# Optimization experiments

Hardware: AMD Instinct MI355X
Metric: run time of the kernel (lower is better)

The kernel has to match this reference:

```python
import jax, jax.numpy as jnp
import numpy as np

V, E, HD, T = 32000, 100, 256, 17   # vocab, embed dim, lstm hidden (bidir total), tagset
B, S = 64, 1024
H = HD // 2                         # per-direction hidden


def setup_inputs() -> dict:
    key = jax.random.key(0)
    ks = jax.random.split(key, 16)
    p = lambda k, sh: (jax.random.normal(k, sh, jnp.float32) * 0.1)
    sentence = jax.random.randint(ks[0], (B, S), 0, V)
    mask = jnp.ones((B, S), dtype=bool)
    embed = p(ks[1], (V, E)).at[0].set(0.0)  # padding_idx=0
    inp = {
        "sentence": sentence,
        "mask": mask,
        "embed": embed,
        "w_ih_f": p(ks[2], (4 * H, E)), "w_hh_f": p(ks[3], (4 * H, H)),
        "b_ih_f": p(ks[4], (4 * H,)), "b_hh_f": p(ks[5], (4 * H,)),
        "w_ih_b": p(ks[6], (4 * H, E)), "w_hh_b": p(ks[7], (4 * H, H)),
        "b_ih_b": p(ks[8], (4 * H,)), "b_hh_b": p(ks[9], (4 * H,)),
        "fc_w": p(ks[10], (T, HD)), "fc_b": p(ks[11], (T,)),
        "start_trans": p(ks[12], (T,)),
        "end_trans": p(ks[13], (T,)),
        "trans": p(ks[14], (T, T)),
    }
    return inp


def _lstm_dir(xs, w_ih, w_hh, b_ih, b_hh):
    # xs: [S, B, E] -> hs: [S, B, H]. PyTorch gate order: i, f, g, o.
    xg = jnp.einsum('sbe,ge->sbg', xs, w_ih) + b_ih  # precompute input projections
    h0 = jnp.zeros((xs.shape[1], H), xs.dtype)
    def step(carry, xg_t):
        h, c = carry
        g = xg_t + h @ w_hh.T + b_hh
        i, f, gg, o = jnp.split(g, 4, axis=-1)
        c = jax.nn.sigmoid(f) * c + jax.nn.sigmoid(i) * jnp.tanh(gg)
        h = jax.nn.sigmoid(o) * jnp.tanh(c)
        return (h, c), h
    _, hs = jax.lax.scan(step, (h0, h0), xg)
    return hs


def _emissions(sentence, embed, w_ih_f, w_hh_f, b_ih_f, b_hh_f,
               w_ih_b, w_hh_b, b_ih_b, b_hh_b, fc_w, fc_b):
    x = embed[sentence]                      # [B, S, E] (dropout is identity in eval)
    xs = x.transpose(1, 0, 2)                # [S, B, E]
    hf = _lstm_dir(xs, w_ih_f, w_hh_f, b_ih_f, b_hh_f)
    hb = _lstm_dir(xs[::-1], w_ih_b, w_hh_b, b_ih_b, b_hh_b)[::-1]
    hcat = jnp.concatenate([hf, hb], axis=-1)            # [S, B, 2H]
    return jnp.einsum('sbh,th->sbt', hcat, fc_w) + fc_b  # [S, B, T]


def reference(sentence, mask, embed, w_ih_f, w_hh_f, b_ih_f, b_hh_f,
              w_ih_b, w_hh_b, b_ih_b, b_hh_b, fc_w, fc_b,
              start_trans, end_trans, trans):
    em = _emissions(sentence, embed, w_ih_f, w_hh_f, b_ih_f, b_hh_f,
                    w_ih_b, w_hh_b, b_ih_b, b_hh_b, fc_w, fc_b)  # [S, B, T]
    mk = mask.T  # [S, B]

    # Viterbi forward pass (max-plus recurrence over the tagset)
    score0 = start_trans + em[0]  # [B, T]
    def vstep(score, inp):
        emit_t, mask_t = inp
        ns = score[:, :, None] + trans[None] + emit_t[:, None, :]  # [B, T_prev, T_cur]
        best = ns.max(axis=1)
        idx = jnp.argmax(ns, axis=1)                                # [B, T]
        score = jnp.where(mask_t[:, None], best, score)
        return score, idx
    score, hist = jax.lax.scan(vstep, score0, (em[1:], mk[1:]))    # hist: [S-1, B, T]
    score = score + end_trans
    last_tag = jnp.argmax(score, axis=-1)                          # [B]

    # Backtrace (mask-aware: frozen past sequence end)
    def back(tag, inp):
        idx_t, mask_t = inp
        prev = jnp.take_along_axis(idx_t, tag[:, None], axis=1)[:, 0]
        tag = jnp.where(mask_t, prev, tag)
        return tag, tag
    _, ys = jax.lax.scan(back, last_tag, (hist, mk[1:]), reverse=True)  # [S-1, B]
    path = jnp.concatenate([ys, last_tag[None]], axis=0).T              # [B, S]
    return path
```

## Files before the change

### kernel.cpp

```cpp
#include <hip/hip_runtime.h>
#include <math.h>

#define S_LEN 1024
#define BATCH 64
#define EDIM  100
#define HDIM  128
#define G4    512
#define TAGS  17

typedef __attribute__((ext_vector_type(2))) float f32x2;
typedef __attribute__((ext_vector_type(4))) float f32x4;

__device__ __forceinline__ f32x2 pkfma(f32x2 a, f32x2 b, f32x2 c) {
    return __builtin_elementwise_fma(a, b, c);
}

template<int CTRL>
__device__ __forceinline__ float qperm(float x) {
    int i = __float_as_int(x);
    i = __builtin_amdgcn_update_dpp(0, i, CTRL, 0xF, 0xF, true);
    return __int_as_float(i);
}
#define QX1 qperm<0xB1>
#define QX2 qperm<0x4E>

__device__ __forceinline__ float fast_tanh_u(float x) {
    float e = __expf(-2.f * x);
    return fmaf(2.f, __builtin_amdgcn_rcpf(1.f + e), -1.f);
}

#define RDLANE(v, jj) __int_as_float(__builtin_amdgcn_readlane(__float_as_int(v), (jj)))

#define STEP_BARRIER() do {                                          \
    __builtin_amdgcn_sched_barrier(0);                               \
    asm volatile("s_waitcnt lgkmcnt(0)\n\ts_barrier" ::: "memory");  \
    __builtin_amdgcn_sched_barrier(0);                               \
} while (0)

__global__ __launch_bounds__(512, 1) void fused_scan_proj(
    const float* __restrict__ xgf_s, const float* __restrict__ xgb_s,
    const float* __restrict__ w_hh_f, const float* __restrict__ w_hh_b,
    float* __restrict__ hcat, float* __restrict__ h_state, float* __restrict__ c_state,
    int t0_scan, int clen, int nscan,
    const int* __restrict__ sentence, const float* __restrict__ embed,
    const float* __restrict__ w_ih_f, const float* __restrict__ b_ih_f, const float* __restrict__ b_hh_f,
    const float* __restrict__ w_ih_b, const float* __restrict__ b_ih_b, const float* __restrict__ b_hh_b,
    float* __restrict__ xgf_p, float* __restrict__ xgb_p, int t0_proj, int nproj_n,
    const float* __restrict__ fc_w, const float* __restrict__ fc_b,
    float* __restrict__ em, int fc_t0a, int fc_t0b)
{
    __shared__ __align__(16) float smem[24576];

    if ((int)blockIdx.x < nscan) {
        const int t     = threadIdx.x;
        const int gid   = t >> 2, q = t & 3;
        const int b     = blockIdx.x & 63;
        const int dir   = blockIdx.x >> 6;
        const int chain = blockIdx.x;

        const float* whh = dir ? w_hh_b : w_hh_f;
        f32x2 wl[4][8], wh[4][8];
#pragma unroll
        for (int g4 = 0; g4 < 4; ++g4) {
            const f32x4* wr = (const f32x4*)(whh + (g4 * HDIM + gid) * HDIM + q * 32);
#pragma unroll
            for (int i = 0; i < 8; ++i) {
                f32x4 v = wr[i];
                wl[g4][i] = v.xy;
                wh[g4][i] = v.zw;
            }
        }

        typedef float hl_t[4][36];
        hl_t* h_lds = (hl_t*)smem;
        float c_reg = 0.f;
        if (t0_scan == 0) {
            if (t < HDIM) h_lds[0][t >> 5][t & 31] = 0.f;
        } else {
            c_reg = c_state[chain * HDIM + gid];
            if (t < HDIM) h_lds[0][t >> 5][t & 31] = h_state[chain * HDIM + t];
        }
        __syncthreads();

        const float* xgp = (dir ? xgb_s : xgf_s) + (long)b * G4 + gid * 4;
        float4 z4; z4.x = z4.y = z4.z = z4.w = 0.f;
        float4 xgc = *(const float4*)xgp;
        float4 xgn = (clen > 1) ? *(const float4*)(xgp + (long)BATCH * G4) : z4;

        float* hc_base = hcat + (long)b * S_LEN * 256 + dir * HDIM + gid;
        float hv = 0.f;
        float hbuf[8];

        for (int sb = 0; sb < clen; sb += 8) {
#pragma unroll
            for (int k = 0; k < 8; ++k) {
                const int s = sb + k;
                float4 xg2 = z4;
                if (s + 2 < clen) xg2 = *(const float4*)(xgp + (long)(s + 2) * BATCH * G4);

                const int cur = k & 1;
                const float* hp = &h_lds[cur][q][0];
                f32x2 ac0 = {0.f, 0.f}, ac1 = {0.f, 0.f}, ac2 = {0.f, 0.f}, ac3 = {0.f, 0.f};
#pragma unroll
                for (int i = 0; i < 8; ++i) {
                    f32x4 h4 = *(const f32x4*)(hp + i * 4);
                    f32x2 hlo = h4.xy, hhi = h4.zw;
                    ac0 = pkfma(wl[0][i], hlo, ac0); ac0 = pkfma(wh[0][i], hhi, ac0);
                    ac1 = pkfma(wl[1][i], hlo, ac1); ac1 = pkfma(wh[1][i], hhi, ac1);
                    ac2 = pkfma(wl[2][i], hlo, ac2); ac2 = pkfma(wh[2][i], hhi, ac2);
                    ac3 = pkfma(wl[3][i], hlo, ac3); ac3 = pkfma(wh[3][i], hhi, ac3);
                }
                float a0 = ac0.x + ac0.y, a1 = ac1.x + ac1.y;
                float a2 = ac2.x + ac2.y, a3 = ac3.x + ac3.y;

                a0 += QX1(a0); a1 += QX1(a1); a2 += QX1(a2); a3 += QX1(a3);
                a0 += QX2(a0); a1 += QX2(a1); a2 += QX2(a2); a3 += QX2(a3);

                float av = (q == 0) ? a0 : (q == 1) ? a1 : (q == 2) ? a2 : a3;
                float xv = (q == 0) ? xgc.x : (q == 1) ? xgc.y : (q == 2) ? xgc.z : xgc.w;
                float pre = xv + av;
                float xin = (q == 2) ? 2.f * pre : pre;
                float e   = __expf(-xin);
                float sgm = __builtin_amdgcn_rcpf(1.f + e);
                float act = (q == 2) ? fmaf(2.f, sgm, -1.f) : sgm;
                float t1 = QX1(act);
                float t2 = QX2(act);
                float t3 = QX2(t1);
                float gi = (q == 0) ? act : (q == 1) ? t1 : (q == 2) ? t2 : t3;
                float gf = (q == 1) ? act : (q == 0) ? t1 : (q == 3) ? t2 : t3;
                float gg = (q == 2) ? act : (q == 3) ? t1 : (q == 0) ? t2 : t3;
                float go = (q == 3) ? act : (q == 2) ? t1 : (q == 1) ? t2 : t3;
                c_reg = gf * c_reg + gi * gg;
                hv = go * fast_tanh_u(c_reg);
                hbuf[k] = hv;

                if (q == 0) h_lds[cur ^ 1][gid >> 5][gid & 31] = hv;
                STEP_BARRIER();
                xgc = xgn; xgn = xg2;
            }
            if (q == 0) {
#pragma unroll
                for (int k = 0; k < 8; ++k) {
                    int tg = dir ? (S_LEN - 1 - (t0_scan + sb + k)) : (t0_scan + sb + k);
                    hc_base[(long)tg * 256] = hbuf[k];
                }
            }
        }

        if (q == 0) {
            c_state[chain * HDIM + gid] = c_reg;
            h_state[chain * HDIM + gid] = hv;
        }
    } else if ((int)blockIdx.x < nscan + nproj_n) {
        if (t0_proj < 0) return;
        const int pb   = blockIdx.x - nscan;
        const int tid  = threadIdx.x;
        const int row0 = pb * 16;

        float (*tile_f)[G4] = (float(*)[G4])smem;
        float (*tile_b)[G4] = (float(*)[G4])(smem + 8192);
        float (*xf)[EDIM] = (float(*)[EDIM])(smem + 16384);
        float (*xb)[EDIM] = (float(*)[EDIM])(smem + 16384 + 1600);
        int* tok = (int*)(smem + 16384 + 3200);

        if (tid < 32) {
            int r = tid & 15;
            int row = row0 + r;
            int s = row >> 6, b = row & 63;
            int tt = (tid < 16) ? (t0_proj + s) : (S_LEN - 1 - (t0_proj + s));
            tok[tid] = sentence[b * S_LEN + tt];
        }
        __syncthreads();
        for (int i = tid; i < 16 * EDIM; i += 512) {
            int r = i / EDIM, e = i - r * EDIM;
            xf[r][e] = embed[(long)tok[r] * EDIM + e];
            xb[r][e] = embed[(long)tok[16 + r] * EDIM + e];
        }
        __syncthreads();

        const float* wptr[2];
        float bias[2];
#pragma unroll
        for (int ci = 0; ci < 2; ++ci) {
            int c = tid + 512 * ci;
            if (c < G4) { wptr[ci] = w_ih_f + c * EDIM; bias[ci] = b_ih_f[c] + b_hh_f[c]; }
            else { int cb = c - G4; wptr[ci] = w_ih_b + cb * EDIM; bias[ci] = b_ih_b[cb] + b_hh_b[cb]; }
        }

        float acc[2][16];
#pragma unroll
        for (int ci = 0; ci < 2; ++ci)
#pragma unroll
            for (int r = 0; r < 16; ++r) acc[ci][r] = 0.f;

        for (int e = 0; e < EDIM; e += 4) {
            float4 w4[2];
#pragma unroll
            for (int ci = 0; ci < 2; ++ci) w4[ci] = *(const float4*)(wptr[ci] + e);
#pragma unroll
            for (int r = 0; r < 16; ++r) {
                float4 xvf = *(const float4*)&xf[r][e];
                float4 xvb = *(const float4*)&xb[r][e];
#pragma unroll
                for (int ci = 0; ci < 2; ++ci) {
                    float4 xv = (ci == 0) ? xvf : xvb;
                    acc[ci][r] = fmaf(w4[ci].x, xv.x, acc[ci][r]);
                    acc[ci][r] = fmaf(w4[ci].y, xv.y, acc[ci][r]);
                    acc[ci][r] = fmaf(w4[ci].z, xv.z, acc[ci][r]);
                    acc[ci][r] = fmaf(w4[ci].w, xv.w, acc[ci][r]);
                }
            }
        }

        {
            const int cpos = (tid & 127) * 4 + (tid >> 7);
#pragma unroll
            for (int r = 0; r < 16; ++r) {
                tile_f[r][cpos] = acc[0][r] + bias[0];
                tile_b[r][cpos] = acc[1][r] + bias[1];
            }
        }
        __syncthreads();
        {
            float4*       df = (float4*)(xgf_p + (long)row0 * G4);
            float4*       db = (float4*)(xgb_p + (long)row0 * G4);
            const float4* sf = (const float4*)tile_f;
            const float4* sb4 = (const float4*)tile_b;
            for (int i = tid; i < (16 * G4) / 4; i += 512) {
                df[i] = sf[i];
                db[i] = sb4[i];
            }
        }
    } else {
        const int fcb0 = blockIdx.x - nscan - nproj_n;
        const int nfc1 = clen >> 1;
        int fb, ft0;
        if (fcb0 < nfc1) { fb = fcb0; ft0 = fc_t0a; }
        else             { fb = fcb0 - nfc1; ft0 = fc_t0b; }
        if (ft0 < 0) return;

        const int tid = threadIdx.x;
        float* w_lds = smem;
        float* part  = smem + TAGS * 256;

        for (int i = tid; i < TAGS * 256; i += 512) w_lds[i] = fc_w[i];
        __syncthreads();

        const int r = tid >> 2, p = tid & 3;
        const int idx0 = fb * 128 + r;
        const int b  = idx0 / clen;
        const int i0 = idx0 - b * clen;
        const long row = (long)b * S_LEN + ft0 + i0;
        const float* hrow = hcat + row * 256 + p * 64;

        float acc[TAGS];
#pragma unroll
        for (int tg = 0; tg < TAGS; ++tg) acc[tg] = 0.f;

        for (int e4 = 0; e4 < 16; ++e4) {
            float4 xv = *(const float4*)(hrow + e4 * 4);
            const float* wp = w_lds + p * 64 + e4 * 4;
#pragma unroll
            for (int tg = 0; tg < TAGS; ++tg) {
                acc[tg] = fmaf(xv.x, wp[tg * 256 + 0], acc[tg]);
                acc[tg] = fmaf(xv.y, wp[tg * 256 + 1], acc[tg]);
                acc[tg] = fmaf(xv.z, wp[tg * 256 + 2], acc[tg]);
                acc[tg] = fmaf(xv.w, wp[tg * 256 + 3], acc[tg]);
            }
        }
#pragma unroll
        for (int tg = 0; tg < TAGS; ++tg) part[(r * TAGS + tg) * 4 + p] = acc[tg];
        __syncthreads();

        for (int idx = tid; idx < 128 * TAGS; idx += 512) {
            int rr = idx / TAGS, tg = idx - rr * TAGS;
            const float* pp = part + (rr * TAGS + tg) * 4;
            float v = ((pp[0] + pp[1]) + (pp[2] + pp[3])) + fc_b[tg];
            int ridx = fb * 128 + rr;
            int bb = ridx / clen;
            int ii = ridx - bb * clen;
            em[((long)bb * S_LEN + ft0 + ii) * TAGS + tg] = v;
        }
    }
}

#define MAX3(a,b,c) fmaxf(fmaxf((a),(b)),(c))
#define MIN3(a,b,c) min(min((a),(b)),(c))

__device__ __forceinline__ float max17(const float* a) {
    float m0 = MAX3(a[0], a[1], a[2]);
    float m1 = MAX3(a[3], a[4], a[5]);
    float m2 = MAX3(a[6], a[7], a[8]);
    float m3 = MAX3(a[9], a[10], a[11]);
    float m4 = MAX3(a[12], a[13], a[14]);
    float m5 = fmaxf(a[15], a[16]);
    float n0 = MAX3(m0, m1, m2);
    float n1 = MAX3(m3, m4, m5);
    return fmaxf(n0, n1);
}

__global__ __launch_bounds__(256) void decode_kernel(
    const float* __restrict__ em,
    const float* __restrict__ start_trans, const float* __restrict__ end_trans,
    const float* __restrict__ trans, int* __restrict__ out)
{
    const int b = blockIdx.x;
    const int tid = threadIdx.x;
    __shared__ __align__(16) float e_lds[S_LEN * TAGS];
    __shared__ __align__(16) float s_lds[S_LEN * TAGS];
    __shared__ float s_tr[TAGS * TAGS];
    __shared__ unsigned char hist[S_LEN * TAGS];
    __shared__ int tags[S_LEN];
    __shared__ int lt;

    {
        const float4* ef4 = (const float4*)(em + (long)b * S_LEN * TAGS);
        float4* el4 = (float4*)e_lds;
        for (int i = tid; i < (S_LEN * TAGS) / 4; i += 256) el4[i] = ef4[i];
        for (int i = tid; i < TAGS * TAGS; i += 256) s_tr[i] = trans[i];
    }
    __syncthreads();

    if (tid < 64) {
        const int lane = tid;
        const int cl = (lane < TAGS) ? lane : 0;
        float tcol[TAGS], etr[TAGS];
#pragma unroll
        for (int jj = 0; jj < TAGS; ++jj) {
            tcol[jj] = s_tr[jj * TAGS + cl];
            etr[jj]  = end_trans[jj];
        }

        float sc = start_trans[cl] + e_lds[cl];
        if (lane < TAGS) s_lds[cl] = sc;

        float em_cur = e_lds[1 * TAGS + cl];
#pragma unroll 2
        for (int s = 1; s < S_LEN; ++s) {
            int sn = (s + 1 < S_LEN) ? (s + 1) : s;
            float em_next = e_lds[sn * TAGS + cl];

            float a[TAGS];
#pragma unroll
            for (int jj = 0; jj < TAGS; ++jj)
                a[jj] = RDLANE(sc, jj) + tcol[jj];

            float amax = max17(a);
            sc = amax + em_cur;
            if (lane < TAGS) s_lds[s * TAGS + cl] = sc;
            em_cur = em_next;
        }

        float ev[TAGS];
#pragma unroll
        for (int jj = 0; jj < TAGS; ++jj) ev[jj] = RDLANE(sc, jj) + etr[jj];
        float bestv = max17(ev);
        int c[17];
#pragma unroll
        for (int j = 0; j < 17; ++j) c[j] = (ev[j] == bestv) ? j : 255;
        int m0 = MIN3(c[0], c[1], c[2]);
        int m1 = MIN3(c[3], c[4], c[5]);
        int m2 = MIN3(c[6], c[7], c[8]);
        int m3 = MIN3(c[9], c[10], c[11]);
        int m4 = MIN3(c[12], c[13], c[14]);
        int m5 = min(c[15], c[16]);
        int bt = min(MIN3(m0, m1, m2), MIN3(m3, m4, m5));
        if (lane == 0) lt = bt;
    }
    __syncthreads();

    for (int idx = tid; idx < (S_LEN - 1) * TAGS; idx += 256) {
        int s = idx / TAGS + 1;
        int c = idx - (s - 1) * TAGS;
        const float* sprev = s_lds + (s - 1) * TAGS;
        float emv = e_lds[s * TAGS + c];
        float cur = s_lds[s * TAGS + c];
        int bi = 255;
#pragma unroll
        for (int j = TAGS - 1; j >= 0; --j) {
            float v = (sprev[j] + s_tr[j * TAGS + c]) + emv;
            if (v == cur) bi = j;
        }
        hist[s * TAGS + c] = (unsigned char)bi;
    }
    __syncthreads();

    if (tid == 0) {
        int tag = lt;
        tags[S_LEN - 1] = tag;
        for (int s = S_LEN - 2; s >= 0; --s) {
            tag = hist[(s + 1) * TAGS + tag];
            tags[s] = tag;
        }
    }
    __syncthreads();
    for (int t = tid; t < S_LEN; t += 256) out[b * S_LEN + t] = tags[t];
}

extern "C" void kernel_launch(void* const* d_in, const int* in_sizes, int n_in,
                              void* d_out, int out_size, void* d_ws, size_t ws_size,
                              hipStream_t stream) {
    const int*   sentence    = (const int*)d_in[0];
    const float* embed       = (const float*)d_in[2];
    const float* w_ih_f      = (const float*)d_in[3];
    const float* w_hh_f      = (const float*)d_in[4];
    const float* b_ih_f      = (const float*)d_in[5];
    const float* b_hh_f      = (const float*)d_in[6];
    const float* w_ih_b      = (const float*)d_in[7];
    const float* w_hh_b      = (const float*)d_in[8];
    const float* b_ih_b      = (const float*)d_in[9];
    const float* b_hh_b      = (const float*)d_in[10];
    const float* fc_w        = (const float*)d_in[11];
    const float* fc_b        = (const float*)d_in[12];
    const float* start_trans = (const float*)d_in[13];
    const float* end_trans   = (const float*)d_in[14];
    const float* trans       = (const float*)d_in[15];
    int* out = (int*)d_out;

    const size_t hcat_e = (size_t)S_LEN * BATCH * 256;
    const size_t em_e   = (size_t)S_LEN * BATCH * TAGS;
    const size_t st_e   = (size_t)128 * HDIM;
    const size_t fixed  = hcat_e + em_e + 2 * st_e + 64;
    static const int cands[] = {1024, 512, 256, 128, 64};
    int C = 64;
    for (int ci = 0; ci < 5; ++ci) {
        int nch = S_LEN / cands[ci];
        size_t nbuf = (nch == 1) ? 2 : 4;
        size_t need = (nbuf * (size_t)cands[ci] * BATCH * G4 + fixed) * 4;
        if (need <= ws_size) { C = cands[ci]; break; }
    }
    const int nchunk = S_LEN / C;
    const size_t xg1 = (size_t)C * BATCH * G4;

    float* ws   = (float*)d_ws;
    float* xgf0 = ws;
    float* xgb0 = xgf0 + xg1;
    float* xgf1 = xgb0 + xg1;
    float* xgb1 = (nchunk > 1) ? xgf1 + xg1 : xgb0;
    float* base = (nchunk > 1) ? xgb1 + xg1 : xgf1;
    float* hcat     = base;
    float* em       = hcat + hcat_e;
    float* h_state  = em + em_e;
    float* c_state  = h_state + st_e;

    const int nproj = C * 4;
    const int nfc1  = C / 2;

    fused_scan_proj<<<nproj, 512, 0, stream>>>(
        nullptr, nullptr, w_hh_f, w_hh_b, hcat, h_state, c_state, 0, C, 0,
        sentence, embed, w_ih_f, b_ih_f, b_hh_f, w_ih_b, b_ih_b, b_hh_b,
        xgf0, xgb0, 0, nproj, fc_w, fc_b, em, -1, -1);

    for (int k = 0; k < nchunk; ++k) {
        const bool par1 = (k & 1) != 0;
        float* sf  = par1 ? xgf1 : xgf0;
        float* sbx = par1 ? xgb1 : xgb0;
        float* pf  = par1 ? xgf0 : xgf1;
        float* pbx = par1 ? xgb0 : xgb1;
        const bool hp = (k + 1 < nchunk);
        const int np = hp ? nproj : 0;

        int fca = -1, fcb = -1, nr = 0;
        if (2 * k >= nchunk + 1) {
            int m1 = k - 1, m2 = nchunk - k;
            fca = m1 * C; nr = 1;
            if (m2 != m1) { fcb = m2 * C; nr = 2; }
        }
        const int grid = 128 + np + nr * nfc1;
        fused_scan_proj<<<grid, 512, 0, stream>>>(
            sf, sbx, w_hh_f, w_hh_b, hcat, h_state, c_state, k * C, C, 128,
            sentence, embed, w_ih_f, b_ih_f, b_hh_f, w_ih_b, b_ih_b, b_hh_b,
            pf, pbx, hp ? (k + 1) * C : -1, np,
            fc_w, fc_b, em, fca, fcb);
    }
    {
        int fca = (nchunk - 1) * C;
        int fcb = (nchunk > 1) ? 0 : -1;
        int nr  = (nchunk > 1) ? 2 : 1;
        fused_scan_proj<<<nr * nfc1, 512, 0, stream>>>(
            nullptr, nullptr, w_hh_f, w_hh_b, hcat, h_state, c_state, 0, C, 0,
            sentence, embed, w_ih_f, b_ih_f, b_hh_f, w_ih_b, b_ih_b, b_hh_b,
            nullptr, nullptr, -1, 0, fc_w, fc_b, em, fca, fcb);
    }

    decode_kernel<<<BATCH, 256, 0, stream>>>(
        em, start_trans, end_trans, trans, out);
}
```

Before: 1.046 ms.

## Parallelize Viterbi backtrace with segment tag maps and widen decode block

The serial 1023-step backtrace on one thread is replaced by a three-phase scheme. First, all 17 start tags of each of 64 segments are traced in parallel to build a per-segment tag map. Next, one thread composes those 64 maps into segment boundary tags, and then 64 threads re-trace their segments and write the output directly. The decode block also grows from 256 to 512 threads for the load and history phases. This shortens the serial dependency chain at the cost of redundant tracing work and extra barriers.

```diff
diff --git a/kernel.cpp b/kernel.cpp
--- a/kernel.cpp
+++ b/kernel.cpp
@@ -299,7 +299,7 @@
     return fmaxf(n0, n1);
 }
 
-__global__ __launch_bounds__(256) void decode_kernel(
+__global__ __launch_bounds__(512) void decode_kernel(
     const float* __restrict__ em,
     const float* __restrict__ start_trans, const float* __restrict__ end_trans,
     const float* __restrict__ trans, int* __restrict__ out)
@@ -310,14 +310,15 @@
     __shared__ __align__(16) float s_lds[S_LEN * TAGS];
     __shared__ float s_tr[TAGS * TAGS];
     __shared__ unsigned char hist[S_LEN * TAGS];
-    __shared__ int tags[S_LEN];
+    __shared__ unsigned char maps[64][TAGS];
+    __shared__ int bt[64];
     __shared__ int lt;
 
     {
         const float4* ef4 = (const float4*)(em + (long)b * S_LEN * TAGS);
         float4* el4 = (float4*)e_lds;
-        for (int i = tid; i < (S_LEN * TAGS) / 4; i += 256) el4[i] = ef4[i];
-        for (int i = tid; i < TAGS * TAGS; i += 256) s_tr[i] = trans[i];
+        for (int i = tid; i < (S_LEN * TAGS) / 4; i += 512) el4[i] = ef4[i];
+        for (int i = tid; i < TAGS * TAGS; i += 512) s_tr[i] = trans[i];
     }
     __syncthreads();
 
@@ -364,12 +365,12 @@
         int m3 = MIN3(c[9], c[10], c[11]);
         int m4 = MIN3(c[12], c[13], c[14]);
         int m5 = min(c[15], c[16]);
-        int bt = min(MIN3(m0, m1, m2), MIN3(m3, m4, m5));
-        if (lane == 0) lt = bt;
+        int btag = min(MIN3(m0, m1, m2), MIN3(m3, m4, m5));
+        if (lane == 0) lt = btag;
     }
     __syncthreads();
 
-    for (int idx = tid; idx < (S_LEN - 1) * TAGS; idx += 256) {
+    for (int idx = tid; idx < (S_LEN - 1) * TAGS; idx += 512) {
         int s = idx / TAGS + 1;
         int c = idx - (s - 1) * TAGS;
         const float* sprev = s_lds + (s - 1) * TAGS;
@@ -385,16 +386,33 @@
     }
     __syncthreads();
 
+    for (int task = tid; task < 64 * TAGS; task += 512) {
+        int g = task / TAGS, st = task - g * TAGS;
+        int hi = (g == 63) ? (S_LEN - 1) : (16 * (g + 1));
+        int t = st;
+        for (int r = hi; r > 16 * g; --r) t = hist[r * TAGS + t];
+        maps[g][st] = (unsigned char)t;
+    }
+    __syncthreads();
+
     if (tid == 0) {
-        int tag = lt;
-        tags[S_LEN - 1] = tag;
-        for (int s = S_LEN - 2; s >= 0; --s) {
-            tag = hist[(s + 1) * TAGS + tag];
-            tags[s] = tag;
-        }
+        int t = lt;
+        for (int g = 63; g >= 0; --g) { t = maps[g][t]; bt[g] = t; }
     }
     __syncthreads();
-    for (int t = tid; t < S_LEN; t += 256) out[b * S_LEN + t] = tags[t];
+
+    if (tid < 64) {
+        const int g = tid;
+        int hi = (g == 63) ? (S_LEN - 1) : (16 * (g + 1));
+        int t = (g == 63) ? lt : bt[g + 1];
+        int* ob = out + (long)b * S_LEN;
+        for (int r = hi; r > 16 * g; --r) {
+            t = hist[r * TAGS + t];
+            ob[r - 1] = t;
+        }
+    } else if (tid == 64) {
+        out[(long)b * S_LEN + (S_LEN - 1)] = lt;
+    }
 }
 
 extern "C" void kernel_launch(void* const* d_in, const int* in_sizes, int n_in,
@@ -483,6 +501,6 @@
             nullptr, nullptr, -1, 0, fc_w, fc_b, em, fca, fcb);
     }
 
-    decode_kernel<<<BATCH, 256, 0, stream>>>(
+    decode_kernel<<<BATCH, 512, 0, stream>>>(
         em, start_trans, end_trans, trans, out);
 }
```

After: 1.018 ms. -2.8%, faster.
